# Kernel optimization log

Measured on AMD Instinct MI355X. Metric: run time of the kernel, lower is better.

Reference implementation:

```python
import jax, jax.numpy as jnp
import numpy as np

NEG_INF = -9e15
ALPHA = 0.2  # LeakyReLU negative slope
OUT_FEATURES = 128


def setup_inputs() -> dict:
    key = jax.random.key(0)
    k1, k2, k3, k4 = jax.random.split(key, 4)
    B, N, F_in, F_out = 4, 4096, 256, OUT_FEATURES
    h = jax.random.normal(k1, (B, N, F_in), dtype=jnp.float32)
    adj = jax.random.randint(k2, (B, N, N), 0, 2, dtype=jnp.int32)
    W = jax.random.normal(k3, (F_in, F_out), dtype=jnp.float32) * 0.07
    a = jax.random.normal(k4, (2 * F_out, 1), dtype=jnp.float32) * 0.1
    return {"h": h, "adj": adj, "W": W, "a": a}


def reference(h, adj, W, a):
    # Wh: (B, N, F_out)
    Wh = jnp.einsum('bni,io->bno', h, W)
    a1 = a[:OUT_FEATURES, 0]   # (F_out,)
    a2 = a[OUT_FEATURES:, 0]   # (F_out,)
    Wh1 = Wh @ a1              # (B, N)
    Wh2 = Wh @ a2              # (B, N)
    e = Wh1[:, :, None] + Wh2[:, None, :]          # (B, N, N)
    e = jnp.where(e >= 0, e, ALPHA * e)             # LeakyReLU
    e = jnp.where(adj > 0, e, NEG_INF)              # adjacency mask
    attention = jax.nn.softmax(e, axis=-1)          # (B, N, N)
    # dropout omitted: reference runs in eval mode (training=False)
    h_prime = jnp.einsum('bnm,bmo->bno', attention, Wh)
    return jax.nn.elu(h_prime)  # concat=True
```

## Files before the change

kernel.cpp:

```cpp
#include <hip/hip_runtime.h>
#include <hip/hip_bf16.h>
#include <math.h>

typedef __attribute__((ext_vector_type(4))) float  f32x4;
typedef __attribute__((ext_vector_type(4))) int    i32x4;
typedef __attribute__((ext_vector_type(8))) short  s16x8;
typedef __attribute__((ext_vector_type(4))) short  s16x4;
typedef __attribute__((ext_vector_type(8))) __bf16 bf16x8;

#define LOG2E 1.4426950408889634f

__device__ __forceinline__ short f32_to_bf16_rne(float f) {
    unsigned u = __builtin_bit_cast(unsigned, f);
    u += 0x7fffu + ((u >> 16) & 1u);
    return (short)(u >> 16);
}
__device__ __forceinline__ bf16x8 as_bf16x8(s16x8 v) {
    return __builtin_bit_cast(bf16x8, v);
}

__global__ void k0_wt(const float* __restrict__ W, short* __restrict__ WT) {
    int g = blockIdx.x * 256 + threadIdx.x;
    int col = g >> 6;
    int k0 = (g & 63) * 4;
    s16x4 v;
    #pragma unroll
    for (int i = 0; i < 4; ++i) v[i] = f32_to_bf16_rne(W[(k0 + i) * 128 + col]);
    *(s16x4*)(WT + col * 256 + k0) = v;
}

__global__ __launch_bounds__(256, 2) void k1_gemm(
    const float* __restrict__ h, const float* __restrict__ a,
    const short* __restrict__ WT,
    short* __restrict__ WhT, float* __restrict__ Wh1p, float* __restrict__ Tp)
{
    int l = threadIdx.x & 63;
    int w = threadIdx.x >> 6;
    int gw = blockIdx.x * 4 + w;
    int r0 = gw * 16;
    int lm = l & 15, q = l >> 4;

    f32x4 acc[8];
    #pragma unroll
    for (int ct = 0; ct < 8; ++ct) acc[ct] = (f32x4)0.0f;

    const float* hrow = h + (long)(r0 + lm) * 256;
    for (int kb = 0; kb < 8; ++kb) {
        int kbase = kb * 32 + q * 8;
        f32x4 h0 = *(const f32x4*)(hrow + kbase);
        f32x4 h1 = *(const f32x4*)(hrow + kbase + 4);
        s16x8 af;
        #pragma unroll
        for (int j = 0; j < 4; ++j) af[j] = f32_to_bf16_rne(h0[j]);
        #pragma unroll
        for (int j = 0; j < 4; ++j) af[4 + j] = f32_to_bf16_rne(h1[j]);
        bf16x8 afb = as_bf16x8(af);
        #pragma unroll
        for (int ct = 0; ct < 8; ++ct) {
            s16x8 bf = *(const s16x8*)(WT + (ct * 16 + lm) * 256 + kbase);
            acc[ct] = __builtin_amdgcn_mfma_f32_16x16x32_bf16(afb, as_bf16x8(bf), acc[ct], 0, 0, 0);
        }
    }

    int b = r0 >> 12;
    int nb = r0 & 4095;
    float p1[4] = {0.f, 0.f, 0.f, 0.f}, p2[4] = {0.f, 0.f, 0.f, 0.f};
    #pragma unroll
    for (int ct = 0; ct < 8; ++ct) {
        int col = ct * 16 + lm;
        float a1c = a[col], a2c = a[128 + col];
        s16x4 vv;
        #pragma unroll
        for (int r = 0; r < 4; ++r) {
            float v = acc[ct][r];
            p1[r] += v * a1c;
            p2[r] += v * a2c;
            vv[r] = f32_to_bf16_rne(v);
        }
        *(s16x4*)(WhT + ((long)(b * 128 + col) * 4096 + nb + q * 4)) = vv;
    }
    #pragma unroll
    for (int off = 1; off < 16; off <<= 1) {
        #pragma unroll
        for (int r = 0; r < 4; ++r) {
            p1[r] += __shfl_xor(p1[r], off);
            p2[r] += __shfl_xor(p2[r], off);
        }
    }
    if (lm == 0) {
        #pragma unroll
        for (int r = 0; r < 4; ++r) {
            int row = r0 + q * 4 + r;
            Wh1p[row] = LOG2E * p1[r];
            Tp[row]   = LOG2E * p2[r];
        }
    }
}

__global__ void k2_tmax(const float* __restrict__ Tp, float* __restrict__ Tmax) {
    __shared__ float red[256];
    int b = blockIdx.x, t = threadIdx.x;
    float mx = -1e30f;
    for (int i = 0; i < 16; ++i) mx = fmaxf(mx, Tp[b * 4096 + t + i * 256]);
    red[t] = mx;
    __syncthreads();
    for (int s = 128; s > 0; s >>= 1) {
        if (t < s) red[t] = fmaxf(red[t], red[t + s]);
        __syncthreads();
    }
    if (t == 0) Tmax[b] = red[0];
}

template <int SPLIT, bool DIRECT>
__global__ __launch_bounds__(256, 4) void k3_attn(
    const int* __restrict__ adj, const short* __restrict__ WhT,
    const float* __restrict__ Wh1p, const float* __restrict__ Tp,
    const float* __restrict__ Tmax,
    float* __restrict__ U, float* __restrict__ Z, float* __restrict__ out)
{
    __shared__ __align__(16) short tile[128 * 128];
    int bid = blockIdx.x;
    int mh = bid % SPLIT;
    int nt = (bid / SPLIT) & 63;
    int b  = bid / (SPLIT * 64);
    int n0 = nt * 64;
    int l = threadIdx.x & 63, w = threadIdx.x >> 6;
    int lm = l & 15, q = l >> 4;

    int n_lane = n0 + w * 16 + lm;
    float sp  = Wh1p[b * 4096 + n_lane];
    float xm  = sp + Tmax[b];
    float Mrow = fmaxf(xm, 0.2f * xm);

    const int MTILES = 4096 / (SPLIT * 128);
    int mbase0 = mh * (4096 / SPLIT);

    const int*   adjrow = adj + ((long)(b * 4096 + n_lane) << 12);
    const float* tpb    = Tp + b * 4096;
    const short* whtb   = WhT + (long)b * 128 * 4096;

    f32x4 acc[8];
    #pragma unroll
    for (int ct = 0; ct < 8; ++ct) acc[ct] = (f32x4)0.0f;
    float z = 0.0f;

    #pragma unroll 1
    for (int ti = 0; ti < MTILES; ++ti) {
        int m0 = mbase0 + ti * 128;
        __syncthreads();
        {
            int colw = w * 32;
            #pragma unroll
            for (int j = 0; j < 8; ++j) {
                int cb = colw + j * 4;
                int col = cb + q;
                int gchunk = lm ^ (col & 7);
                const short* gp = whtb + (long)col * 4096 + m0 + gchunk * 8;
                short* lp = tile + cb * 128;
                __builtin_amdgcn_global_load_lds(
                    (const __attribute__((address_space(1))) void*)gp,
                    (__attribute__((address_space(3))) void*)lp,
                    16, 0, 0);
            }
        }
        i32x4 aj[8];
        #pragma unroll
        for (int ks = 0; ks < 4; ++ks) {
            int bm = m0 + ks * 32 + q * 8;
            aj[2 * ks]     = *(const i32x4*)(adjrow + bm);
            aj[2 * ks + 1] = *(const i32x4*)(adjrow + bm + 4);
        }
        __syncthreads();

        #pragma unroll
        for (int ks = 0; ks < 4; ++ks) {
            int bm = m0 + ks * 32 + q * 8;
            f32x4 t0 = *(const f32x4*)(tpb + bm);
            f32x4 t1 = *(const f32x4*)(tpb + bm + 4);
            s16x8 af;
            float zs = 0.0f;
            #pragma unroll
            for (int half = 0; half < 2; ++half) {
                i32x4 a4 = aj[2 * ks + half];
                f32x4 t4 = half ? t1 : t0;
                #pragma unroll
                for (int j = 0; j < 4; ++j) {
                    float y = sp + t4[j];
                    float e = fmaxf(y, 0.2f * y) - Mrow;
                    float wv = __builtin_amdgcn_exp2f(e);
                    wv = (a4[j] != 0) ? wv : 0.0f;
                    zs += wv;
                    af[half * 4 + j] = f32_to_bf16_rne(wv);
                }
            }
            z += zs;
            bf16x8 afb = as_bf16x8(af);
            #pragma unroll
            for (int ct = 0; ct < 8; ++ct) {
                int col = ct * 16 + lm;
                int pos = (ks * 4 + q) ^ (col & 7);
                s16x8 bf = *(const s16x8*)(tile + col * 128 + pos * 8);
                acc[ct] = __builtin_amdgcn_mfma_f32_16x16x32_bf16(afb, as_bf16x8(bf), acc[ct], 0, 0, 0);
            }
        }
    }

    z += __shfl_xor(z, 16);
    z += __shfl_xor(z, 32);

    if (DIRECT) {
        float zr[4];
        #pragma unroll
        for (int r = 0; r < 4; ++r) zr[r] = __shfl(z, q * 4 + r);
        float* orow = out + (long)(b * 4096 + n0 + w * 16) * 128;
        #pragma unroll
        for (int ct = 0; ct < 8; ++ct) {
            int col = ct * 16 + lm;
            #pragma unroll
            for (int r = 0; r < 4; ++r) {
                float x = acc[ct][r] / zr[r];
                orow[(q * 4 + r) * 128 + col] = (x > 0.f) ? x : (expf(x) - 1.0f);
            }
        }
    } else {
        if (l < 16) Z[(b * SPLIT + mh) * 4096 + n0 + w * 16 + lm] = z;
        float* ub = U + ((long)(b * SPLIT + mh) * 4096 + n0 + w * 16) * 128;
        #pragma unroll
        for (int ct = 0; ct < 8; ++ct) {
            int col = ct * 16 + lm;
            #pragma unroll
            for (int r = 0; r < 4; ++r)
                ub[(q * 4 + r) * 128 + col] = acc[ct][r];
        }
    }
}

__global__ void k4_combine(const float* __restrict__ U, const float* __restrict__ Z,
                           float* __restrict__ out) {
    long g = (long)blockIdx.x * 256 + threadIdx.x;
    long off = g * 4;
    long nf = off >> 7;
    int b = (int)(nf >> 12), n = (int)(nf & 4095), col = (int)(off & 127);
    const long slice = (long)4096 * 128;
    long base0 = ((long)(b * 4) * 4096 + n) * 128 + col;
    f32x4 s = (f32x4)0.0f;
    float zz = 0.0f;
    #pragma unroll
    for (int i = 0; i < 4; ++i) {
        f32x4 u = *(const f32x4*)(U + base0 + i * slice);
        s += u;
        zz += Z[(b * 4 + i) * 4096 + n];
    }
    f32x4 v;
    #pragma unroll
    for (int i = 0; i < 4; ++i) {
        float x = s[i] / zz;
        v[i] = (x > 0.f) ? x : (expf(x) - 1.0f);
    }
    *(f32x4*)(out + off) = v;
}

extern "C" void kernel_launch(void* const* d_in, const int* in_sizes, int n_in,
                              void* d_out, int out_size, void* d_ws, size_t ws_size,
                              hipStream_t stream) {
    const float* h   = (const float*)d_in[0];
    const int*   adj = (const int*)d_in[1];
    const float* W   = (const float*)d_in[2];
    const float* a   = (const float*)d_in[3];
    float* out = (float*)d_out;

    char* ws = (char*)d_ws;
    short* WhT  = (short*)ws;
    short* WT   = (short*)(ws + 4194304);
    float* Wh1p = (float*)(ws + 4259840);
    float* Tp   = (float*)(ws + 4325376);
    float* Tmax = (float*)(ws + 4390912);
    float* U    = (float*)(ws + 4391168);
    float* Z    = (float*)(ws + 4391168 + 33554432);

    k0_wt<<<32, 256, 0, stream>>>(W, WT);
    k1_gemm<<<256, 256, 0, stream>>>(h, a, WT, WhT, Wh1p, Tp);
    k2_tmax<<<4, 256, 0, stream>>>(Tp, Tmax);

    bool split4 = ws_size >= (size_t)(4391168 + 33554432 + 262144);
    if (split4) {
        k3_attn<4, false><<<1024, 256, 0, stream>>>(adj, WhT, Wh1p, Tp, Tmax, U, Z, out);
        k4_combine<<<2048, 256, 0, stream>>>(U, Z, out);
    } else {
        k3_attn<1, true><<<256, 256, 0, stream>>>(adj, WhT, Wh1p, Tp, Tmax, nullptr, nullptr, out);
    }
    (void)in_sizes; (void)n_in; (void)out_size;
}
```

Baseline: 435.9 us.

## Restructure attention kernel: per-wave M-split, register double-buffering, no LDS

The attention kernel now gives each block 32 rows, and each of its four waves handles its own quarter of the neighbour dimension, so the split now lives inside a block rather than across blocks. WhT fragments are loaded straight from global memory into registers, with two chunks in flight in a software pipeline, which removes the LDS tile and both __syncthreads per tile. Each wave computes two 16-row MFMA groups, so every B fragment it loads is used twice. This costs more registers (launch bounds drop to 2 blocks per CU) and repeats WhT reads across blocks through the cache. The unsplit fallback path is removed and the workspace-size check is dropped.

```diff
diff --git a/kernel.cpp b/kernel.cpp
--- a/kernel.cpp
+++ b/kernel.cpp
@@ -111,126 +111,121 @@
     if (t == 0) Tmax[b] = red[0];
 }
 
-template <int SPLIT, bool DIRECT>
-__global__ __launch_bounds__(256, 4) void k3_attn(
+template <int SPLIT>
+__global__ __launch_bounds__(256, 2) void k3_attn(
     const int* __restrict__ adj, const short* __restrict__ WhT,
     const float* __restrict__ Wh1p, const float* __restrict__ Tp,
     const float* __restrict__ Tmax,
-    float* __restrict__ U, float* __restrict__ Z, float* __restrict__ out)
+    float* __restrict__ U, float* __restrict__ Z)
 {
-    __shared__ __align__(16) short tile[128 * 128];
-    int bid = blockIdx.x;
-    int mh = bid % SPLIT;
-    int nt = (bid / SPLIT) & 63;
-    int b  = bid / (SPLIT * 64);
-    int n0 = nt * 64;
     int l = threadIdx.x & 63, w = threadIdx.x >> 6;
     int lm = l & 15, q = l >> 4;
-
-    int n_lane = n0 + w * 16 + lm;
-    float sp  = Wh1p[b * 4096 + n_lane];
-    float xm  = sp + Tmax[b];
-    float Mrow = fmaxf(xm, 0.2f * xm);
-
-    const int MTILES = 4096 / (SPLIT * 128);
-    int mbase0 = mh * (4096 / SPLIT);
-
-    const int*   adjrow = adj + ((long)(b * 4096 + n_lane) << 12);
-    const float* tpb    = Tp + b * 4096;
-    const short* whtb   = WhT + (long)b * 128 * 4096;
-
-    f32x4 acc[8];
-    #pragma unroll
-    for (int ct = 0; ct < 8; ++ct) acc[ct] = (f32x4)0.0f;
-    float z = 0.0f;
-
+    int bid = blockIdx.x;
+    int b  = bid >> 7;
+    int rg = bid & 127;
+    int r0 = rg * 32;
+    int mh = w;
+    const int MSLICE = 4096 / SPLIT;
+    const int CHUNKS = MSLICE / 32;
+    int M0 = mh * MSLICE;
+
+    int row0 = r0 + lm, row1 = r0 + 16 + lm;
+    float sp0 = Wh1p[b * 4096 + row0];
+    float sp1 = Wh1p[b * 4096 + row1];
+    float tmx = Tmax[b];
+    float xm0 = sp0 + tmx, xm1 = sp1 + tmx;
+    float M0r = fmaxf(xm0, 0.2f * xm0);
+    float M1r = fmaxf(xm1, 0.2f * xm1);
+
+    const int*   adjr0 = adj + ((long)(b * 4096 + row0) << 12) + q * 8;
+    const int*   adjr1 = adj + ((long)(b * 4096 + row1) << 12) + q * 8;
+    const float* tpb   = Tp + b * 4096 + q * 8;
+    const short* whtb  = WhT + (long)b * 128 * 4096 + q * 8 + lm * 4096;
+
+    f32x4 acc0[8], acc1[8];
+    #pragma unroll
+    for (int ct = 0; ct < 8; ++ct) { acc0[ct] = (f32x4)0.0f; acc1[ct] = (f32x4)0.0f; }
+    float z0 = 0.0f, z1 = 0.0f;
+
+    struct Chunk {
+        s16x8 bf[8];
+        i32x4 a0[2], a1[2];
+        f32x4 t[2];
+    };
+
+    auto loadChunk = [&](Chunk& c, int m0) {
+        #pragma unroll
+        for (int ct = 0; ct < 8; ++ct)
+            c.bf[ct] = *(const s16x8*)(whtb + ct * 16 * 4096 + m0);
+        c.a0[0] = *(const i32x4*)(adjr0 + m0);
+        c.a0[1] = *(const i32x4*)(adjr0 + m0 + 4);
+        c.a1[0] = *(const i32x4*)(adjr1 + m0);
+        c.a1[1] = *(const i32x4*)(adjr1 + m0 + 4);
+        c.t[0]  = *(const f32x4*)(tpb + m0);
+        c.t[1]  = *(const f32x4*)(tpb + m0 + 4);
+    };
+
+    auto computeChunk = [&](Chunk& c) {
+        s16x8 a0f, a1f;
+        float zz0 = 0.0f, zz1 = 0.0f;
+        #pragma unroll
+        for (int half = 0; half < 2; ++half) {
+            i32x4 m0v = c.a0[half], m1v = c.a1[half];
+            f32x4 t4 = c.t[half];
+            #pragma unroll
+            for (int j = 0; j < 4; ++j) {
+                float tt = t4[j];
+                float y0 = sp0 + tt;
+                float e0 = fmaxf(y0, 0.2f * y0) - M0r;
+                float w0 = __builtin_amdgcn_exp2f(e0);
+                w0 = (m0v[j] != 0) ? w0 : 0.0f;
+                zz0 += w0;
+                a0f[half * 4 + j] = f32_to_bf16_rne(w0);
+                float y1 = sp1 + tt;
+                float e1 = fmaxf(y1, 0.2f * y1) - M1r;
+                float w1 = __builtin_amdgcn_exp2f(e1);
+                w1 = (m1v[j] != 0) ? w1 : 0.0f;
+                zz1 += w1;
+                a1f[half * 4 + j] = f32_to_bf16_rne(w1);
+            }
+        }
+        z0 += zz0; z1 += zz1;
+        bf16x8 a0b = as_bf16x8(a0f), a1b = as_bf16x8(a1f);
+        #pragma unroll
+        for (int ct = 0; ct < 8; ++ct) {
+            bf16x8 bb = as_bf16x8(c.bf[ct]);
+            acc0[ct] = __builtin_amdgcn_mfma_f32_16x16x32_bf16(a0b, bb, acc0[ct], 0, 0, 0);
+            acc1[ct] = __builtin_amdgcn_mfma_f32_16x16x32_bf16(a1b, bb, acc1[ct], 0, 0, 0);
+        }
+    };
+
+    Chunk cA, cB;
+    loadChunk(cA, M0);
     #pragma unroll 1
-    for (int ti = 0; ti < MTILES; ++ti) {
-        int m0 = mbase0 + ti * 128;
-        __syncthreads();
-        {
-            int colw = w * 32;
-            #pragma unroll
-            for (int j = 0; j < 8; ++j) {
-                int cb = colw + j * 4;
-                int col = cb + q;
-                int gchunk = lm ^ (col & 7);
-                const short* gp = whtb + (long)col * 4096 + m0 + gchunk * 8;
-                short* lp = tile + cb * 128;
-                __builtin_amdgcn_global_load_lds(
-                    (const __attribute__((address_space(1))) void*)gp,
-                    (__attribute__((address_space(3))) void*)lp,
-                    16, 0, 0);
-            }
-        }
-        i32x4 aj[8];
-        #pragma unroll
-        for (int ks = 0; ks < 4; ++ks) {
-            int bm = m0 + ks * 32 + q * 8;
-            aj[2 * ks]     = *(const i32x4*)(adjrow + bm);
-            aj[2 * ks + 1] = *(const i32x4*)(adjrow + bm + 4);
-        }
-        __syncthreads();
-
-        #pragma unroll
-        for (int ks = 0; ks < 4; ++ks) {
-            int bm = m0 + ks * 32 + q * 8;
-            f32x4 t0 = *(const f32x4*)(tpb + bm);
-            f32x4 t1 = *(const f32x4*)(tpb + bm + 4);
-            s16x8 af;
-            float zs = 0.0f;
-            #pragma unroll
-            for (int half = 0; half < 2; ++half) {
-                i32x4 a4 = aj[2 * ks + half];
-                f32x4 t4 = half ? t1 : t0;
-                #pragma unroll
-                for (int j = 0; j < 4; ++j) {
-                    float y = sp + t4[j];
-                    float e = fmaxf(y, 0.2f * y) - Mrow;
-                    float wv = __builtin_amdgcn_exp2f(e);
-                    wv = (a4[j] != 0) ? wv : 0.0f;
-                    zs += wv;
-                    af[half * 4 + j] = f32_to_bf16_rne(wv);
-                }
-            }
-            z += zs;
-            bf16x8 afb = as_bf16x8(af);
-            #pragma unroll
-            for (int ct = 0; ct < 8; ++ct) {
-                int col = ct * 16 + lm;
-                int pos = (ks * 4 + q) ^ (col & 7);
-                s16x8 bf = *(const s16x8*)(tile + col * 128 + pos * 8);
-                acc[ct] = __builtin_amdgcn_mfma_f32_16x16x32_bf16(afb, as_bf16x8(bf), acc[ct], 0, 0, 0);
-            }
-        }
-    }
-
-    z += __shfl_xor(z, 16);
-    z += __shfl_xor(z, 32);
-
-    if (DIRECT) {
-        float zr[4];
-        #pragma unroll
-        for (int r = 0; r < 4; ++r) zr[r] = __shfl(z, q * 4 + r);
-        float* orow = out + (long)(b * 4096 + n0 + w * 16) * 128;
-        #pragma unroll
-        for (int ct = 0; ct < 8; ++ct) {
-            int col = ct * 16 + lm;
-            #pragma unroll
-            for (int r = 0; r < 4; ++r) {
-                float x = acc[ct][r] / zr[r];
-                orow[(q * 4 + r) * 128 + col] = (x > 0.f) ? x : (expf(x) - 1.0f);
-            }
-        }
-    } else {
-        if (l < 16) Z[(b * SPLIT + mh) * 4096 + n0 + w * 16 + lm] = z;
-        float* ub = U + ((long)(b * SPLIT + mh) * 4096 + n0 + w * 16) * 128;
-        #pragma unroll
-        for (int ct = 0; ct < 8; ++ct) {
-            int col = ct * 16 + lm;
-            #pragma unroll
-            for (int r = 0; r < 4; ++r)
-                ub[(q * 4 + r) * 128 + col] = acc[ct][r];
+    for (int c = 0; c < CHUNKS; c += 2) {
+        loadChunk(cB, M0 + (c + 1) * 32);
+        computeChunk(cA);
+        int m2 = (c + 2 < CHUNKS) ? M0 + (c + 2) * 32 : M0;
+        loadChunk(cA, m2);
+        computeChunk(cB);
+    }
+
+    z0 += __shfl_xor(z0, 16); z0 += __shfl_xor(z0, 32);
+    z1 += __shfl_xor(z1, 16); z1 += __shfl_xor(z1, 32);
+
+    int slice = b * SPLIT + mh;
+    if (l < 16) {
+        Z[slice * 4096 + r0 + lm]      = z0;
+        Z[slice * 4096 + r0 + 16 + lm] = z1;
+    }
+    float* ub = U + ((long)slice * 4096 + r0) * 128;
+    #pragma unroll
+    for (int ct = 0; ct < 8; ++ct) {
+        int col = ct * 16 + lm;
+        #pragma unroll
+        for (int r = 0; r < 4; ++r) {
+            ub[(q * 4 + r) * 128 + col]        = acc0[ct][r];
+            ub[(16 + q * 4 + r) * 128 + col]   = acc1[ct][r];
         }
     }
 }
@@ -281,13 +276,7 @@
     k0_wt<<<32, 256, 0, stream>>>(W, WT);
     k1_gemm<<<256, 256, 0, stream>>>(h, a, WT, WhT, Wh1p, Tp);
     k2_tmax<<<4, 256, 0, stream>>>(Tp, Tmax);
-
-    bool split4 = ws_size >= (size_t)(4391168 + 33554432 + 262144);
-    if (split4) {
-        k3_attn<4, false><<<1024, 256, 0, stream>>>(adj, WhT, Wh1p, Tp, Tmax, U, Z, out);
-        k4_combine<<<2048, 256, 0, stream>>>(U, Z, out);
-    } else {
-        k3_attn<1, true><<<256, 256, 0, stream>>>(adj, WhT, Wh1p, Tp, Tmax, nullptr, nullptr, out);
-    }
-    (void)in_sizes; (void)n_in; (void)out_size;
-}
+    k3_attn<4><<<512, 256, 0, stream>>>(adj, WhT, Wh1p, Tp, Tmax, U, Z);
+    k4_combine<<<2048, 256, 0, stream>>>(U, Z, out);
+    (void)in_sizes; (void)n_in; (void)out_size; (void)ws_size;
+}
```

After: 528.8 us. 21.3% more time.
